# Performance work log

Hardware: AMD Instinct MI355X
Metric: run time of the kernel (lower is better)

The kernel has to match this reference:

```python
import jax, jax.numpy as jnp
import numpy as np

N_NODES = 50000
N_EDGES = 320000
HIDDEN = 256
EDGE_DIM = 64
NUM_HEADS = 8
HEAD_DIM = HIDDEN // NUM_HEADS


def setup_inputs() -> dict:
    key = jax.random.key(0)
    ks = jax.random.split(key, 9)
    s = HIDDEN ** -0.5
    return {
        "x": jax.random.normal(ks[0], (N_NODES, HIDDEN), dtype=jnp.float32),
        "edge_index": jax.random.randint(ks[1], (2, N_EDGES), 0, N_NODES, dtype=jnp.int64),
        "edge_attr": jax.random.normal(ks[2], (N_EDGES, EDGE_DIM), dtype=jnp.float32),
        "Wq": jax.random.normal(ks[3], (HIDDEN, HIDDEN), dtype=jnp.float32) * s,
        "Wk": jax.random.normal(ks[4], (HIDDEN, HIDDEN), dtype=jnp.float32) * s,
        "Wv": jax.random.normal(ks[5], (HIDDEN, HIDDEN), dtype=jnp.float32) * s,
        "We": jax.random.normal(ks[6], (EDGE_DIM, NUM_HEADS), dtype=jnp.float32) * (EDGE_DIM ** -0.5),
        "Wo": jax.random.normal(ks[7], (HIDDEN, HIDDEN), dtype=jnp.float32) * s,
        "bo": jnp.zeros((HIDDEN,), dtype=jnp.float32),
    }


def reference(x, edge_index, edge_attr, Wq, Wk, Wv, We, Wo, bo):
    N = x.shape[0]
    # node projections -> (N, H, Dh)
    Q = (x @ Wq).reshape(N, NUM_HEADS, HEAD_DIM)
    K = (x @ Wk).reshape(N, NUM_HEADS, HEAD_DIM)
    V = (x @ Wv).reshape(N, NUM_HEADS, HEAD_DIM)
    src, tgt = edge_index[0], edge_index[1]
    Q_src = Q[src]   # (E, H, Dh)
    K_tgt = K[tgt]
    V_tgt = V[tgt]
    scale = jnp.float32(HEAD_DIM ** -0.5)
    # per-edge, per-head scores with edge bias: (E, H)
    score = (Q_src * K_tgt).sum(axis=-1) * scale + edge_attr @ We
    # segment softmax over tgt (all heads at once)
    m = jax.ops.segment_max(score, tgt, num_segments=N)          # (N, H)
    ex = jnp.exp(score - m[tgt])                                  # (E, H)
    den = jax.ops.segment_sum(ex, tgt, num_segments=N)           # (N, H)
    attn = ex / den[tgt]                                          # (E, H)
    # weighted scatter-add of V per head -> (N, H, Dh)
    agg = jax.ops.segment_sum(attn[:, :, None] * V_tgt, tgt, num_segments=N)
    out = agg.reshape(N, HIDDEN) @ Wo + bo
    return out
```

## Files before the change

### kernel.cpp

```cpp
#include <hip/hip_runtime.h>
#include <hip/hip_bf16.h>

#define NN 50000
#define NE 320000
#define HID 256
#define NBLK_FLAG 1250
#define NBLK_W2   512
#define FLAG_MAGIC 0x7F3A9C51

typedef __attribute__((ext_vector_type(8))) short bf16x8;
typedef __attribute__((ext_vector_type(4))) float f32x4;

static __device__ __forceinline__ short f2bf(float f) {
    union { __hip_bfloat16 h; short s; } u;
    u.h = __float2bfloat16(f);
    return u.s;
}

__global__ void prep_k(const int* __restrict__ ei, int* __restrict__ flags,
                       const float* __restrict__ Wv, const float* __restrict__ Wo,
                       unsigned short* __restrict__ wsB) {
    const int b = blockIdx.x;
    const int tid = threadIdx.x;
    if (b < NBLK_FLAG) {
        __shared__ int nz;
        if (tid == 0) nz = 0;
        __syncthreads();
        unsigned hv = ((const unsigned*)ei)[2 * tid + 1];
        if (hv != 0u) nz = 1;
        __syncthreads();
        const int is64 = (nz == 0);
        const int e = b * 256 + tid;
        if (e < NE) {
            int t = is64 ? ei[2 * (NE + e)] : ei[NE + e];
            if (t >= 0 && t < NN) flags[t] = FLAG_MAGIC;
        }
    } else {
        __shared__ float part[256];
        const int w  = b - NBLK_FLAG;
        const int i  = w >> 1;
        const int jh = w & 1;
        const int j  = jh * 128 + (tid & 127);
        const int h  = tid >> 7;
        const float* wv = Wv + i * HID + h * 128;
        const float* wo = Wo + (size_t)h * 128 * HID + j;
        float s0 = 0.f, s1 = 0.f, s2 = 0.f, s3 = 0.f;
        #pragma unroll 4
        for (int k = 0; k < 128; k += 4) {
            s0 = fmaf(wv[k + 0], wo[(k + 0) * HID], s0);
            s1 = fmaf(wv[k + 1], wo[(k + 1) * HID], s1);
            s2 = fmaf(wv[k + 2], wo[(k + 2) * HID], s2);
            s3 = fmaf(wv[k + 3], wo[(k + 3) * HID], s3);
        }
        part[tid] = (s0 + s1) + (s2 + s3);
        __syncthreads();
        if (h == 0) {
            const float acc = part[tid] + part[tid + 128];
            const int kt = i >> 6, kp = i & 63;
            const int kk = kp >> 5, hh = (kp >> 3) & 3, e = kp & 7;
            wsB[(kt * 32768 + (j >> 4) * 2048 + kk * 1024 + hh * 256 + (j & 15) * 16 + e * 2) >> 1]
                = (unsigned short)f2bf(acc);
        }
    }
}


#define CS_STRIDE 260

__global__ __launch_bounds__(256, 4) void out_gemm_k(
    const float* __restrict__ x, const unsigned short* __restrict__ wsB,
    const float* __restrict__ bo, const int* __restrict__ flags,
    float* __restrict__ out)
{
    __shared__ char lds[16640];
    float* Cs = (float*)lds;

    const int tid  = threadIdx.x;
    const int wave = tid >> 6;
    const int lane = tid & 63;
    const int rl   = lane & 15;
    const int hi   = lane >> 4;
    const int row0 = blockIdx.x * 32;
    const int wcol = wave * 64;

    const char* gB = (const char*)wsB + wave * 8192 + lane * 16;
    bf16x8 bfrag[4][2];
    #pragma unroll
    for (int n = 0; n < 4; ++n)
        #pragma unroll
        for (int kk = 0; kk < 2; ++kk)
            bfrag[n][kk] = *(const bf16x8*)(gB + n * 2048 + kk * 1024);
    float bov[4];
    #pragma unroll
    for (int n = 0; n < 4; ++n) bov[n] = bo[wcol + n * 16 + rl];

    const int ar = tid >> 3;
    const int aq = tid & 7;
    int grow = row0 + ar; if (grow >= NN) grow = NN - 1;
    const float* asrc = x + (size_t)grow * HID + aq * 8;
    const int swr = (aq ^ (ar & 7)) << 4;

    {
        f32x4 av[8];
        #pragma unroll
        for (int kt = 0; kt < 4; ++kt) {
            av[2 * kt]     = *(const f32x4*)(asrc + kt * 64);
            av[2 * kt + 1] = *(const f32x4*)(asrc + kt * 64 + 4);
        }
        #pragma unroll
        for (int kt = 0; kt < 4; ++kt) {
            const f32x4 v0 = av[2 * kt], v1 = av[2 * kt + 1];
            bf16x8 w;
            w[0] = f2bf(v0[0]); w[1] = f2bf(v0[1]); w[2] = f2bf(v0[2]); w[3] = f2bf(v0[3]);
            w[4] = f2bf(v1[0]); w[5] = f2bf(v1[1]); w[6] = f2bf(v1[2]); w[7] = f2bf(v1[3]);
            *(bf16x8*)(lds + kt * 4096 + ar * 128 + swr) = w;
        }
    }

    __syncthreads();

    f32x4 acc[2][4];
    #pragma unroll
    for (int m = 0; m < 2; ++m)
        #pragma unroll
        for (int n = 0; n < 4; ++n)
            acc[m][n] = (f32x4){0.f, 0.f, 0.f, 0.f};

    int4 flg[2];

    #pragma unroll
    for (int kt = 0; kt < 4; ++kt) {
        #pragma unroll
        for (int kk = 0; kk < 2; ++kk) {
            bf16x8 af[2];
            #pragma unroll
            for (int m = 0; m < 2; ++m)
                af[m] = *(const bf16x8*)(lds + kt * 4096 + (m * 16 + rl) * 128
                                         + ((((kk << 2) + hi) ^ (rl & 7)) << 4));
            #pragma unroll
            for (int m = 0; m < 2; ++m)
                #pragma unroll
                for (int n = 0; n < 4; ++n)
                    acc[m][n] = __builtin_amdgcn_mfma_f32_16x16x32_bf16(af[m], bfrag[n][kk], acc[m][n], 0, 0, 0);
        }
        if (kt < 3) {
            #pragma unroll
            for (int n = 0; n < 4; ++n)
                #pragma unroll
                for (int kk = 0; kk < 2; ++kk)
                    bfrag[n][kk] = *(const bf16x8*)(gB + (kt + 1) * 32768 + n * 2048 + kk * 1024);
        } else {
            #pragma unroll
            for (int m = 0; m < 2; ++m)
                flg[m] = *(const int4*)(flags + row0 + m * 16 + hi * 4);
        }
    }

    #pragma unroll
    for (int h2 = 0; h2 < 2; ++h2) {
        __syncthreads();
        const int fl[4] = {flg[h2].x, flg[h2].y, flg[h2].z, flg[h2].w};
        #pragma unroll
        for (int j = 0; j < 4; ++j) {
            const float msk = (fl[j] == FLAG_MAGIC) ? 1.f : 0.f;
            float* crow = Cs + (hi * 4 + j) * CS_STRIDE + wcol + rl;
            #pragma unroll
            for (int n = 0; n < 4; ++n)
                crow[n * 16] = fmaf(msk, acc[h2][n][j], bov[n]);
        }
        __syncthreads();
        #pragma unroll
        for (int i = 0; i < 4; ++i) {
            const int rloc = wave * 4 + i;
            const f32x4 v = *(const f32x4*)(Cs + rloc * CS_STRIDE + lane * 4);
            const int r = row0 + h2 * 16 + rloc;
            if (r < NN)
                *(f32x4*)(out + (size_t)r * HID + lane * 4) = v;
        }
    }
}


extern "C" void kernel_launch(void* const* d_in, const int* in_sizes, int n_in,
                              void* d_out, int out_size, void* d_ws, size_t ws_size,
                              hipStream_t stream) {
    const float* x   = (const float*)d_in[0];
    const int*   ei  = (const int*)d_in[1];
    const float* Wv  = (const float*)d_in[5];
    const float* Wo  = (const float*)d_in[7];
    const float* bo  = (const float*)d_in[8];
    float* out = (float*)d_out;

    unsigned short* wsB = (unsigned short*)d_ws;
    int* flags = (int*)((char*)d_ws + 4 * 32768);

    prep_k<<<NBLK_FLAG + NBLK_W2, 256, 0, stream>>>(ei, flags, Wv, Wo, wsB);

    dim3 grid((NN + 31) / 32);
    out_gemm_k<<<grid, 256, 0, stream>>>(x, wsB, bo, flags, out);
}
```

Measured before the change: 33.08 us.

## Process two 32-row tiles per block with both A tiles staged upfront

Each block of the output GEMM now covers 64 rows instead of 32, which halves the grid. Both x tiles are loaded and converted to bf16 in LDS before any compute, and the B fragments are reloaded for the second tile. The epilogue staging buffer drops its padded stride and now reuses the first tile's LDS region. The aim is to amortise per-block setup (B fragment and bias loads) and raise memory-level parallelism. The cost is a larger LDS footprint, which may lower occupancy, and possible LDS bank conflicts from the unpadded stride.

Result: slower. 35.79 us (+8.2%).

```diff
diff --git a/kernel.cpp b/kernel.cpp
--- a/kernel.cpp
+++ b/kernel.cpp
@@ -65,14 +65,14 @@
 }
 
 
-#define CS_STRIDE 260
+#define CS_STRIDE 256
 
 __global__ __launch_bounds__(256, 4) void out_gemm_k(
     const float* __restrict__ x, const unsigned short* __restrict__ wsB,
     const float* __restrict__ bo, const int* __restrict__ flags,
     float* __restrict__ out)
 {
-    __shared__ char lds[16640];
+    __shared__ char lds[32768];
     float* Cs = (float*)lds;
 
     const int tid  = threadIdx.x;
@@ -80,8 +80,40 @@
     const int lane = tid & 63;
     const int rl   = lane & 15;
     const int hi   = lane >> 4;
-    const int row0 = blockIdx.x * 32;
+    const int row0 = blockIdx.x * 64;
     const int wcol = wave * 64;
+
+    const int ar = tid >> 3;
+    const int aq = tid & 7;
+    int g0 = row0 + ar;      if (g0 >= NN) g0 = NN - 1;
+    int g1 = row0 + 32 + ar; if (g1 >= NN) g1 = NN - 1;
+    const float* a0 = x + (size_t)g0 * HID + aq * 8;
+    const float* a1 = x + (size_t)g1 * HID + aq * 8;
+    const int swr = (aq ^ (ar & 7)) << 4;
+
+    {
+        f32x4 av[16];
+        #pragma unroll
+        for (int kt = 0; kt < 4; ++kt) {
+            av[2 * kt]     = *(const f32x4*)(a0 + kt * 64);
+            av[2 * kt + 1] = *(const f32x4*)(a0 + kt * 64 + 4);
+        }
+        #pragma unroll
+        for (int kt = 0; kt < 4; ++kt) {
+            av[8 + 2 * kt] = *(const f32x4*)(a1 + kt * 64);
+            av[9 + 2 * kt] = *(const f32x4*)(a1 + kt * 64 + 4);
+        }
+        #pragma unroll
+        for (int t = 0; t < 2; ++t)
+            #pragma unroll
+            for (int kt = 0; kt < 4; ++kt) {
+                const f32x4 v0 = av[t * 8 + 2 * kt], v1 = av[t * 8 + 2 * kt + 1];
+                bf16x8 w;
+                w[0] = f2bf(v0[0]); w[1] = f2bf(v0[1]); w[2] = f2bf(v0[2]); w[3] = f2bf(v0[3]);
+                w[4] = f2bf(v1[0]); w[5] = f2bf(v1[1]); w[6] = f2bf(v1[2]); w[7] = f2bf(v1[3]);
+                *(bf16x8*)(lds + t * 16384 + kt * 4096 + ar * 128 + swr) = w;
+            }
+    }
 
     const char* gB = (const char*)wsB + wave * 8192 + lane * 16;
     bf16x8 bfrag[4][2];
@@ -94,88 +126,77 @@
     #pragma unroll
     for (int n = 0; n < 4; ++n) bov[n] = bo[wcol + n * 16 + rl];
 
-    const int ar = tid >> 3;
-    const int aq = tid & 7;
-    int grow = row0 + ar; if (grow >= NN) grow = NN - 1;
-    const float* asrc = x + (size_t)grow * HID + aq * 8;
-    const int swr = (aq ^ (ar & 7)) << 4;
-
-    {
-        f32x4 av[8];
+    __syncthreads();
+
+    #pragma unroll
+    for (int t = 0; t < 2; ++t) {
+        const int trow0 = row0 + t * 32;
+
+        f32x4 acc[2][4];
+        #pragma unroll
+        for (int m = 0; m < 2; ++m)
+            #pragma unroll
+            for (int n = 0; n < 4; ++n)
+                acc[m][n] = (f32x4){0.f, 0.f, 0.f, 0.f};
+
+        int4 flg[2];
+
         #pragma unroll
         for (int kt = 0; kt < 4; ++kt) {
-            av[2 * kt]     = *(const f32x4*)(asrc + kt * 64);
-            av[2 * kt + 1] = *(const f32x4*)(asrc + kt * 64 + 4);
-        }
-        #pragma unroll
-        for (int kt = 0; kt < 4; ++kt) {
-            const f32x4 v0 = av[2 * kt], v1 = av[2 * kt + 1];
-            bf16x8 w;
-            w[0] = f2bf(v0[0]); w[1] = f2bf(v0[1]); w[2] = f2bf(v0[2]); w[3] = f2bf(v0[3]);
-            w[4] = f2bf(v1[0]); w[5] = f2bf(v1[1]); w[6] = f2bf(v1[2]); w[7] = f2bf(v1[3]);
-            *(bf16x8*)(lds + kt * 4096 + ar * 128 + swr) = w;
-        }
-    }
-
-    __syncthreads();
-
-    f32x4 acc[2][4];
-    #pragma unroll
-    for (int m = 0; m < 2; ++m)
-        #pragma unroll
-        for (int n = 0; n < 4; ++n)
-            acc[m][n] = (f32x4){0.f, 0.f, 0.f, 0.f};
-
-    int4 flg[2];
-
-    #pragma unroll
-    for (int kt = 0; kt < 4; ++kt) {
-        #pragma unroll
-        for (int kk = 0; kk < 2; ++kk) {
-            bf16x8 af[2];
-            #pragma unroll
-            for (int m = 0; m < 2; ++m)
-                af[m] = *(const bf16x8*)(lds + kt * 4096 + (m * 16 + rl) * 128
-                                         + ((((kk << 2) + hi) ^ (rl & 7)) << 4));
-            #pragma unroll
-            for (int m = 0; m < 2; ++m)
+            #pragma unroll
+            for (int kk = 0; kk < 2; ++kk) {
+                bf16x8 af[2];
+                #pragma unroll
+                for (int m = 0; m < 2; ++m)
+                    af[m] = *(const bf16x8*)(lds + t * 16384 + kt * 4096 + (m * 16 + rl) * 128
+                                             + ((((kk << 2) + hi) ^ (rl & 7)) << 4));
+                #pragma unroll
+                for (int m = 0; m < 2; ++m)
+                    #pragma unroll
+                    for (int n = 0; n < 4; ++n)
+                        acc[m][n] = __builtin_amdgcn_mfma_f32_16x16x32_bf16(af[m], bfrag[n][kk], acc[m][n], 0, 0, 0);
+            }
+            if (kt < 3) {
                 #pragma unroll
                 for (int n = 0; n < 4; ++n)
-                    acc[m][n] = __builtin_amdgcn_mfma_f32_16x16x32_bf16(af[m], bfrag[n][kk], acc[m][n], 0, 0, 0);
-        }
-        if (kt < 3) {
-            #pragma unroll
-            for (int n = 0; n < 4; ++n)
-                #pragma unroll
-                for (int kk = 0; kk < 2; ++kk)
-                    bfrag[n][kk] = *(const bf16x8*)(gB + (kt + 1) * 32768 + n * 2048 + kk * 1024);
-        } else {
-            #pragma unroll
-            for (int m = 0; m < 2; ++m)
-                flg[m] = *(const int4*)(flags + row0 + m * 16 + hi * 4);
-        }
-    }
-
-    #pragma unroll
-    for (int h2 = 0; h2 < 2; ++h2) {
-        __syncthreads();
-        const int fl[4] = {flg[h2].x, flg[h2].y, flg[h2].z, flg[h2].w};
-        #pragma unroll
-        for (int j = 0; j < 4; ++j) {
-            const float msk = (fl[j] == FLAG_MAGIC) ? 1.f : 0.f;
-            float* crow = Cs + (hi * 4 + j) * CS_STRIDE + wcol + rl;
-            #pragma unroll
-            for (int n = 0; n < 4; ++n)
-                crow[n * 16] = fmaf(msk, acc[h2][n][j], bov[n]);
-        }
-        __syncthreads();
-        #pragma unroll
-        for (int i = 0; i < 4; ++i) {
-            const int rloc = wave * 4 + i;
-            const f32x4 v = *(const f32x4*)(Cs + rloc * CS_STRIDE + lane * 4);
-            const int r = row0 + h2 * 16 + rloc;
-            if (r < NN)
-                *(f32x4*)(out + (size_t)r * HID + lane * 4) = v;
+                    #pragma unroll
+                    for (int kk = 0; kk < 2; ++kk)
+                        bfrag[n][kk] = *(const bf16x8*)(gB + (kt + 1) * 32768 + n * 2048 + kk * 1024);
+            } else {
+                #pragma unroll
+                for (int m = 0; m < 2; ++m)
+                    flg[m] = *(const int4*)(flags + trow0 + m * 16 + hi * 4);
+                if (t == 0) {
+                    #pragma unroll
+                    for (int n = 0; n < 4; ++n)
+                        #pragma unroll
+                        for (int kk = 0; kk < 2; ++kk)
+                            bfrag[n][kk] = *(const bf16x8*)(gB + n * 2048 + kk * 1024);
+                }
+            }
+        }
+
+        #pragma unroll
+        for (int h2 = 0; h2 < 2; ++h2) {
+            __syncthreads();
+            const int fl[4] = {flg[h2].x, flg[h2].y, flg[h2].z, flg[h2].w};
+            #pragma unroll
+            for (int j = 0; j < 4; ++j) {
+                const float msk = (fl[j] == FLAG_MAGIC) ? 1.f : 0.f;
+                float* crow = Cs + (hi * 4 + j) * CS_STRIDE + wcol + rl;
+                #pragma unroll
+                for (int n = 0; n < 4; ++n)
+                    crow[n * 16] = fmaf(msk, acc[h2][n][j], bov[n]);
+            }
+            __syncthreads();
+            #pragma unroll
+            for (int i = 0; i < 4; ++i) {
+                const int rloc = wave * 4 + i;
+                const f32x4 v = *(const f32x4*)(Cs + rloc * CS_STRIDE + lane * 4);
+                const int r = trow0 + h2 * 16 + rloc;
+                if (r < NN)
+                    *(f32x4*)(out + (size_t)r * HID + lane * 4) = v;
+            }
         }
     }
 }
@@ -196,6 +217,6 @@
 
     prep_k<<<NBLK_FLAG + NBLK_W2, 256, 0, stream>>>(ei, flags, Wv, Wo, wsB);
 
-    dim3 grid((NN + 31) / 32);
+    dim3 grid((NN + 63) / 64);
     out_gemm_k<<<grid, 256, 0, stream>>>(x, wsB, bo, flags, out);
 }
```
